# Kernel optimization log

Measured on AMD Instinct MI355X. Metric: run time of the kernel, lower is better.

## Reference

```python
import jax, jax.numpy as jnp
import numpy as np

B, T, I, H = 2048, 1024, 1, 20


def setup_inputs() -> dict:
    key = jax.random.key(0)
    ks = jax.random.split(key, 7)
    std = 0.01  # matches nn.init.normal_(p, mean=0.0, std=0.01)
    X = jax.random.normal(ks[0], (B, T, I), jnp.float32)
    hidden_prev = jnp.zeros((1, B, H), jnp.float32)
    W_ih = jax.random.normal(ks[1], (3 * H, I), jnp.float32) * std
    W_hh = jax.random.normal(ks[2], (3 * H, H), jnp.float32) * std
    b_ih = jax.random.normal(ks[3], (3 * H,), jnp.float32) * std
    b_hh = jax.random.normal(ks[4], (3 * H,), jnp.float32) * std
    W_out = jax.random.normal(ks[5], (1, H), jnp.float32) * std
    b_out = jax.random.normal(ks[6], (1,), jnp.float32) * std
    return dict(X=X, hidden_prev=hidden_prev, W_ih=W_ih, W_hh=W_hh,
                b_ih=b_ih, b_hh=b_hh, W_out=W_out, b_out=b_out)


def _gru(X, h0, W_ih, W_hh, b_ih, b_hh):
    # Precompute all input projections in one big GEMM: [T, B, 3H]
    gi = jnp.einsum('bti,gi->tbg', X, W_ih) + b_ih

    def step(h, gi_t):
        gh = h @ W_hh.T + b_hh                      # [B, 3H]
        i_r, i_z, i_n = jnp.split(gi_t, 3, axis=-1)  # PyTorch gate order: r, z, n
        h_r, h_z, h_n = jnp.split(gh, 3, axis=-1)
        r = jax.nn.sigmoid(i_r + h_r)
        z = jax.nn.sigmoid(i_z + h_z)
        n = jnp.tanh(i_n + r * h_n)
        h_new = (1.0 - z) * n + z * h
        return h_new, h_new

    h_last, outs = jax.lax.scan(step, h0, gi)        # outs: [T, B, H]
    return jnp.transpose(outs, (1, 0, 2)), h_last    # [B, T, H], [B, H]


def reference(X, hidden_prev, W_ih, W_hh, b_ih, b_hh, W_out, b_out):
    out, h_last = _gru(X, hidden_prev[0], W_ih, W_hh, b_ih, b_hh)
    y = out.reshape(-1, H) @ W_out.T + b_out         # [B*T, 1]
    return y[None], h_last[None]                     # [1, B*T, 1], [1, B, H]
```

## Files before the change

### kernel.cpp

```cpp
#include <hip/hip_runtime.h>


#define LOG2E 1.44269504088896340736f

static __device__ __forceinline__ float fast_rcp(float x) {
    return __builtin_amdgcn_rcpf(x);
}
static __device__ __forceinline__ float fast_exp2(float x) {
    float r;
    asm("v_exp_f32 %0, %1" : "=v"(r) : "v"(x));
    return r;
}
static __device__ __forceinline__ float lane_bcast(float v, int srclane) {
    return __int_as_float(__builtin_amdgcn_readlane(__float_as_int(v), srclane));
}

__global__ __launch_bounds__(64) void gru_fused(
    const float* __restrict__ X,
    const float* __restrict__ H0,
    const float* __restrict__ Wih,
    const float* __restrict__ Whh,
    const float* __restrict__ Bih,
    const float* __restrict__ Bhh,
    const float* __restrict__ Wout,
    const float* __restrict__ Bout,
    float* __restrict__ Y,
    float* __restrict__ Hlast)
{
    constexpr int T = 1024;
    constexpr int H = 20;
    const int b    = blockIdx.x;
    const int lane = threadIdx.x;

    __shared__ float lds[128];

    float w[H];
    float wih_full = 0.f, bihv = 0.f, cbias = 0.f, wih_rz = 0.f;
    if (lane < 60) {
        const float sc = (lane < 40) ? LOG2E : 2.0f * LOG2E;
        #pragma unroll
        for (int k = 0; k < H; ++k) w[k] = Whh[lane * H + k] * sc;
        wih_full = Wih[lane];
        bihv     = Bih[lane];
        if (lane < 40) {
            cbias  = (Bih[lane] + Bhh[lane]) * sc;
            wih_rz = wih_full * sc;
        } else {
            cbias     = Bhh[lane] * sc;
            wih_full *= sc;
            bihv     *= sc;
        }
    } else if (lane == 60) {
        #pragma unroll
        for (int k = 0; k < H; ++k) w[k] = Wout[k];
        cbias = Bout[0];
    } else {
        #pragma unroll
        for (int k = 0; k < H; ++k) w[k] = 0.f;
    }

    const bool is_n = (lane >= 40) && (lane < 60);
    const int  jn   = lane - 40;

    float hcur  = H0[b * H + (is_n ? jn : 0)];

    const int sr = is_n ? jn          : lane;
    const int sz = is_n ? (lane + -20) : lane;

    const float4* X4 = (const float4*)(X + (size_t)b * T);
    float4 xq = X4[0];

    for (int q = 0; q < T / 4; ++q) {
        float4 xn = X4[(q < T / 4 - 1) ? (q + 1) : (T / 4 - 1)];
        #pragma unroll
        for (int u = 0; u < 4; ++u) {
            const int   i = 4 * q + u;
            const float x = (u == 0) ? xq.x : (u == 1) ? xq.y
                          : (u == 2) ? xq.z : xq.w;

            if (u == 1 && (q & 15) == 0 && q > 0) {
                Y[(size_t)b * T + (4 * q - 64) + lane] = lds[lane];
            }

            float hs[H];
            #pragma unroll
            for (int k = 0; k < H; ++k) hs[k] = lane_bcast(hcur, 40 + k);

            float acc  = fmaf(x, wih_rz, cbias);
            float gi   = fmaf(x, wih_full, bihv);
            float acc2 = 0.f;
            #pragma unroll
            for (int k = 0; k < 10; ++k)  acc  = fmaf(hs[k], w[k], acc);
            #pragma unroll
            for (int k = 10; k < 20; ++k) acc2 = fmaf(hs[k], w[k], acc2);
            acc += acc2;

            float s = fast_rcp(1.f + fast_exp2(-acc));

            float rj = __shfl(s, sr, 64);
            float zj = __shfl(s, sz, 64);

            float npre = fmaf(rj, acc, gi);
            float nval = 1.f - 2.f * fast_rcp(1.f + fast_exp2(npre));
            float hnew = fmaf(zj, hcur - nval, nval);
            hcur = hnew;

            const int   waddr = (lane == 60) ? ((i + 63) & 63) : (64 + lane);
            const float wval  = (lane == 60) ? acc : 0.f;
            lds[waddr] = wval;
        }
        xq = xn;
    }

    {
        float hs[H];
        #pragma unroll
        for (int k = 0; k < H; ++k) hs[k] = lane_bcast(hcur, 40 + k);
        float acc  = cbias;
        float acc2 = 0.f;
        #pragma unroll
        for (int k = 0; k < 10; ++k)  acc  = fmaf(hs[k], w[k], acc);
        #pragma unroll
        for (int k = 10; k < 20; ++k) acc2 = fmaf(hs[k], w[k], acc2);
        acc += acc2;
        const int   waddr = (lane == 60) ? 63 : (64 + lane);
        const float wval  = (lane == 60) ? acc : 0.f;
        lds[waddr] = wval;
        Y[(size_t)b * T + (T - 64) + lane] = lds[lane];
    }

    if (is_n) Hlast[b * H + jn] = hcur;
}

extern "C" void kernel_launch(void* const* d_in, const int* in_sizes, int n_in,
                              void* d_out, int out_size, void* d_ws, size_t ws_size,
                              hipStream_t stream) {
    const float* X    = (const float*)d_in[0];
    const float* H0   = (const float*)d_in[1];
    const float* Wih  = (const float*)d_in[2];
    const float* Whh  = (const float*)d_in[3];
    const float* Bih  = (const float*)d_in[4];
    const float* Bhh  = (const float*)d_in[5];
    const float* Wout = (const float*)d_in[6];
    const float* Bout = (const float*)d_in[7];

    constexpr int B = 2048, T = 1024, H = 20;
    float* Y     = (float*)d_out;
    float* Hlast = Y + (size_t)B * T;

    gru_fused<<<dim3(B), dim3(64), 0, stream>>>(X, H0, Wih, Whh, Bih, Bhh,
                                                Wout, Bout, Y, Hlast);
}
```

Before: 309.7 us.

## Process two batch rows per wavefront to interleave independent GRU recurrences

Each 64-lane block now advances two independent batch sequences through the recurrence, issuing both steps back to back inside the unrolled inner loop. The grid is halved and the LDS staging buffer for Y grows to hold both sequences' outputs. The intent is to hide the serial latency of readlane broadcasts, exp/rcp and shuffles by giving the compiler two independent dependency chains per wave, instead of relying on the hardware to switch between two separate waves. The trade-off is higher register pressure, and fewer total waves, which may leave SIMDs with less latency hiding if the compiler does not interleave the two chains well.

```diff
diff --git a/kernel.cpp b/kernel.cpp
--- a/kernel.cpp
+++ b/kernel.cpp
@@ -15,7 +15,50 @@
     return __int_as_float(__builtin_amdgcn_readlane(__float_as_int(v), srclane));
 }
 
-__global__ __launch_bounds__(64) void gru_fused(
+static __device__ __forceinline__ float gru_step(
+    float x, float& hcur, const float* __restrict__ w,
+    float wih_rz, float wih_full, float bihv, float cbias,
+    int sr, int sz)
+{
+    float hs[20];
+    #pragma unroll
+    for (int k = 0; k < 20; ++k) hs[k] = lane_bcast(hcur, 40 + k);
+
+    float acc  = fmaf(x, wih_rz, cbias);
+    float gi   = fmaf(x, wih_full, bihv);
+    float acc2 = 0.f;
+    #pragma unroll
+    for (int k = 0; k < 10; ++k)  acc  = fmaf(hs[k], w[k], acc);
+    #pragma unroll
+    for (int k = 10; k < 20; ++k) acc2 = fmaf(hs[k], w[k], acc2);
+    acc += acc2;
+
+    float s  = fast_rcp(1.f + fast_exp2(-acc));
+    float rj = __shfl(s, sr, 64);
+    float zj = __shfl(s, sz, 64);
+
+    float npre = fmaf(rj, acc, gi);
+    float nval = 1.f - 2.f * fast_rcp(1.f + fast_exp2(npre));
+    hcur = fmaf(zj, hcur - nval, nval);
+    return acc;
+}
+
+static __device__ __forceinline__ float tail_dot(
+    float hcur, const float* __restrict__ w, float cbias)
+{
+    float hs[20];
+    #pragma unroll
+    for (int k = 0; k < 20; ++k) hs[k] = lane_bcast(hcur, 40 + k);
+    float acc  = cbias;
+    float acc2 = 0.f;
+    #pragma unroll
+    for (int k = 0; k < 10; ++k)  acc  = fmaf(hs[k], w[k], acc);
+    #pragma unroll
+    for (int k = 10; k < 20; ++k) acc2 = fmaf(hs[k], w[k], acc2);
+    return acc + acc2;
+}
+
+__global__ __launch_bounds__(64) void gru_fused2(
     const float* __restrict__ X,
     const float* __restrict__ H0,
     const float* __restrict__ Wih,
@@ -29,10 +72,11 @@
 {
     constexpr int T = 1024;
     constexpr int H = 20;
-    const int b    = blockIdx.x;
+    const int b0   = blockIdx.x * 2;
+    const int b1   = b0 + 1;
     const int lane = threadIdx.x;
 
-    __shared__ float lds[128];
+    __shared__ float lds[192];
 
     float w[H];
     float wih_full = 0.f, bihv = 0.f, cbias = 0.f, wih_rz = 0.f;
@@ -61,75 +105,60 @@
 
     const bool is_n = (lane >= 40) && (lane < 60);
     const int  jn   = lane - 40;
+    const int  sr   = is_n ? jn          : lane;
+    const int  sz   = is_n ? (lane - 20) : lane;
 
-    float hcur  = H0[b * H + (is_n ? jn : 0)];
+    float hA = H0[b0 * H + (is_n ? jn : 0)];
+    float hB = H0[b1 * H + (is_n ? jn : 0)];
 
-    const int sr = is_n ? jn          : lane;
-    const int sz = is_n ? (lane + -20) : lane;
+    const float4* X4A = (const float4*)(X + (size_t)b0 * T);
+    const float4* X4B = (const float4*)(X + (size_t)b1 * T);
+    float4 xqA = X4A[0], xqB = X4B[0];
 
-    const float4* X4 = (const float4*)(X + (size_t)b * T);
-    float4 xq = X4[0];
+    float* YA = Y + (size_t)b0 * T;
+    float* YB = Y + (size_t)b1 * T;
 
     for (int q = 0; q < T / 4; ++q) {
-        float4 xn = X4[(q < T / 4 - 1) ? (q + 1) : (T / 4 - 1)];
+        const int qn = (q < T / 4 - 1) ? (q + 1) : (T / 4 - 1);
+        float4 xnA = X4A[qn];
+        float4 xnB = X4B[qn];
         #pragma unroll
         for (int u = 0; u < 4; ++u) {
-            const int   i = 4 * q + u;
-            const float x = (u == 0) ? xq.x : (u == 1) ? xq.y
-                          : (u == 2) ? xq.z : xq.w;
+            const int   i  = 4 * q + u;
+            const float xA = (u == 0) ? xqA.x : (u == 1) ? xqA.y
+                           : (u == 2) ? xqA.z : xqA.w;
+            const float xB = (u == 0) ? xqB.x : (u == 1) ? xqB.y
+                           : (u == 2) ? xqB.z : xqB.w;
 
             if (u == 1 && (q & 15) == 0 && q > 0) {
-                Y[(size_t)b * T + (4 * q - 64) + lane] = lds[lane];
+                YA[(4 * q - 64) + lane] = lds[lane];
+                YB[(4 * q - 64) + lane] = lds[64 + lane];
             }
 
-            float hs[H];
-            #pragma unroll
-            for (int k = 0; k < H; ++k) hs[k] = lane_bcast(hcur, 40 + k);
+            float accA = gru_step(xA, hA, w, wih_rz, wih_full, bihv, cbias, sr, sz);
+            float accB = gru_step(xB, hB, w, wih_rz, wih_full, bihv, cbias, sr, sz);
 
-            float acc  = fmaf(x, wih_rz, cbias);
-            float gi   = fmaf(x, wih_full, bihv);
-            float acc2 = 0.f;
-            #pragma unroll
-            for (int k = 0; k < 10; ++k)  acc  = fmaf(hs[k], w[k], acc);
-            #pragma unroll
-            for (int k = 10; k < 20; ++k) acc2 = fmaf(hs[k], w[k], acc2);
-            acc += acc2;
-
-            float s = fast_rcp(1.f + fast_exp2(-acc));
-
-            float rj = __shfl(s, sr, 64);
-            float zj = __shfl(s, sz, 64);
-
-            float npre = fmaf(rj, acc, gi);
-            float nval = 1.f - 2.f * fast_rcp(1.f + fast_exp2(npre));
-            float hnew = fmaf(zj, hcur - nval, nval);
-            hcur = hnew;
-
-            const int   waddr = (lane == 60) ? ((i + 63) & 63) : (64 + lane);
-            const float wval  = (lane == 60) ? acc : 0.f;
-            lds[waddr] = wval;
+            const int slot = (i + 63) & 63;
+            lds[(lane == 60) ? slot        : (128 + lane)] = accA;
+            lds[(lane == 60) ? (64 + slot) : (128 + lane)] = accB;
         }
-        xq = xn;
+        xqA = xnA;
+        xqB = xnB;
     }
 
     {
-        float hs[H];
-        #pragma unroll
-        for (int k = 0; k < H; ++k) hs[k] = lane_bcast(hcur, 40 + k);
-        float acc  = cbias;
-        float acc2 = 0.f;
-        #pragma unroll
-        for (int k = 0; k < 10; ++k)  acc  = fmaf(hs[k], w[k], acc);
-        #pragma unroll
-        for (int k = 10; k < 20; ++k) acc2 = fmaf(hs[k], w[k], acc2);
-        acc += acc2;
-        const int   waddr = (lane == 60) ? 63 : (64 + lane);
-        const float wval  = (lane == 60) ? acc : 0.f;
-        lds[waddr] = wval;
-        Y[(size_t)b * T + (T - 64) + lane] = lds[lane];
+        float accA = tail_dot(hA, w, cbias);
+        float accB = tail_dot(hB, w, cbias);
+        lds[(lane == 60) ? 63  : (128 + lane)] = accA;
+        lds[(lane == 60) ? 127 : (128 + lane)] = accB;
+        YA[(T - 64) + lane] = lds[lane];
+        YB[(T - 64) + lane] = lds[64 + lane];
     }
 
-    if (is_n) Hlast[b * H + jn] = hcur;
+    if (is_n) {
+        Hlast[b0 * H + jn] = hA;
+        Hlast[b1 * H + jn] = hB;
+    }
 }
 
 extern "C" void kernel_launch(void* const* d_in, const int* in_sizes, int n_in,
@@ -148,6 +177,6 @@
     float* Y     = (float*)d_out;
     float* Hlast = Y + (size_t)B * T;
 
-    gru_fused<<<dim3(B), dim3(64), 0, stream>>>(X, H0, Wih, Whh, Bih, Bhh,
-                                                Wout, Bout, Y, Hlast);
+    gru_fused2<<<dim3(B / 2), dim3(64), 0, stream>>>(X, H0, Wih, Whh, Bih, Bhh,
+                                                     Wout, Bout, Y, Hlast);
 }
```

After: 351.3 us. +13.4%, slower.

## Pack r/n and z/Wout gate rows into paired lanes using v_pk_fma_f32

Applied to the files above, without the earlier changes.

Each lane now holds two gate rows as float2 weight pairs: r with n in lanes 0-19, and z with the output projection in lanes 32-51. The recurrent matvec uses packed FP32 FMAs with the broadcast hidden state duplicated into SGPR pairs, and the accumulation is split across four chains. This removes one of the two cross-lane shuffles per step and shortens the serial critical path per timestep. The cost is hand-written inline asm and a more complex lane mapping, so correctness depends on the lane-to-gate index arithmetic being right.

```diff
diff --git a/kernel.cpp b/kernel.cpp
--- a/kernel.cpp
+++ b/kernel.cpp
@@ -3,19 +3,43 @@
 
 #define LOG2E 1.44269504088896340736f
 
+typedef float f32x2 __attribute__((ext_vector_type(2)));
+
 static __device__ __forceinline__ float fast_rcp(float x) {
     return __builtin_amdgcn_rcpf(x);
 }
-static __device__ __forceinline__ float fast_exp2(float x) {
-    float r;
-    asm("v_exp_f32 %0, %1" : "=v"(r) : "v"(x));
-    return r;
+static __device__ __forceinline__ float exp2neg(float x) {
+    float r; asm("v_exp_f32 %0, -%1" : "=v"(r) : "v"(x)); return r;
 }
-static __device__ __forceinline__ float lane_bcast(float v, int srclane) {
-    return __int_as_float(__builtin_amdgcn_readlane(__float_as_int(v), srclane));
+static __device__ __forceinline__ float exp2pos(float x) {
+    float r; asm("v_exp_f32 %0, %1" : "=v"(r) : "v"(x)); return r;
+}
+static __device__ __forceinline__ unsigned long long dup_sgpr(unsigned int u) {
+    return (((unsigned long long)u) << 32) | (unsigned long long)u;
+}
+static __device__ __forceinline__ void pk_fma_acc(f32x2& acc, f32x2 w,
+                                                  unsigned long long hp) {
+    asm("v_pk_fma_f32 %0, %1, %2, %0" : "+v"(acc) : "v"(w), "s"(hp));
+}
+static __device__ __forceinline__ f32x2 pk_mul(f32x2 w, unsigned long long hp) {
+    f32x2 d; asm("v_pk_mul_f32 %0, %1, %2" : "=v"(d) : "v"(w), "s"(hp));
+    return d;
+}
+static __device__ __forceinline__ f32x2 pk_fma3(f32x2 xf, unsigned long long xp,
+                                                f32x2 cb) {
+    f32x2 d;
+    asm("v_pk_fma_f32 %0, %1, %2, %3" : "=v"(d) : "v"(xf), "s"(xp), "v"(cb));
+    return d;
+}
+static __device__ __forceinline__ f32x2 pk_add(f32x2 a, f32x2 b) {
+    f32x2 d; asm("v_pk_add_f32 %0, %1, %2" : "=v"(d) : "v"(a), "v"(b));
+    return d;
+}
+static __device__ __forceinline__ int rfl(float v) {
+    return __builtin_amdgcn_readfirstlane(__float_as_int(v));
 }
 
-__global__ __launch_bounds__(64) void gru_fused(
+__global__ __launch_bounds__(64) void gru_pk(
     const float* __restrict__ X,
     const float* __restrict__ H0,
     const float* __restrict__ Wih,
@@ -34,102 +58,117 @@
 
     __shared__ float lds[128];
 
-    float w[H];
-    float wih_full = 0.f, bihv = 0.f, cbias = 0.f, wih_rz = 0.f;
-    if (lane < 60) {
-        const float sc = (lane < 40) ? LOG2E : 2.0f * LOG2E;
+    f32x2 w[H];
+    f32x2 cb = {0.f, 0.f}, xf = {0.f, 0.f};
+    float wihn2 = 0.f, bihn2 = 0.f;
+    if (lane < 20) {
         #pragma unroll
-        for (int k = 0; k < H; ++k) w[k] = Whh[lane * H + k] * sc;
-        wih_full = Wih[lane];
-        bihv     = Bih[lane];
-        if (lane < 40) {
-            cbias  = (Bih[lane] + Bhh[lane]) * sc;
-            wih_rz = wih_full * sc;
-        } else {
-            cbias     = Bhh[lane] * sc;
-            wih_full *= sc;
-            bihv     *= sc;
-        }
-    } else if (lane == 60) {
+        for (int k = 0; k < H; ++k)
+            w[k] = f32x2{Whh[lane * H + k] * LOG2E,
+                         Whh[(40 + lane) * H + k] * (2.f * LOG2E)};
+        cb    = f32x2{(Bih[lane] + Bhh[lane]) * LOG2E,
+                      Bhh[40 + lane] * (2.f * LOG2E)};
+        xf    = f32x2{Wih[lane] * LOG2E, 0.f};
+        wihn2 = Wih[40 + lane] * (2.f * LOG2E);
+        bihn2 = Bih[40 + lane] * (2.f * LOG2E);
+    } else if (lane >= 32 && lane < 52) {
+        const int j = lane - 32;
         #pragma unroll
-        for (int k = 0; k < H; ++k) w[k] = Wout[k];
-        cbias = Bout[0];
+        for (int k = 0; k < H; ++k)
+            w[k] = f32x2{Whh[(20 + j) * H + k] * LOG2E,
+                         (j == 0) ? Wout[k] : 0.f};
+        cb = f32x2{(Bih[20 + j] + Bhh[20 + j]) * LOG2E,
+                   (j == 0) ? Bout[0] : 0.f};
+        xf = f32x2{Wih[20 + j] * LOG2E, 0.f};
     } else {
         #pragma unroll
-        for (int k = 0; k < H; ++k) w[k] = 0.f;
+        for (int k = 0; k < H; ++k) w[k] = f32x2{0.f, 0.f};
     }
 
-    const bool is_n = (lane >= 40) && (lane < 60);
-    const int  jn   = lane - 40;
+    const bool isy = (lane == 32);
+    const int  ztr = (lane < 32) ? (lane + 32) : lane;
 
-    float hcur  = H0[b * H + (is_n ? jn : 0)];
-
-    const int sr = is_n ? jn          : lane;
-    const int sz = is_n ? (lane + -20) : lane;
+    float hcur = H0[b * H + ((lane < 20) ? lane : 0)];
 
     const float4* X4 = (const float4*)(X + (size_t)b * T);
     float4 xq = X4[0];
 
     for (int q = 0; q < T / 4; ++q) {
-        float4 xn = X4[(q < T / 4 - 1) ? (q + 1) : (T / 4 - 1)];
+        const int qn = (q < T / 4 - 1) ? (q + 1) : (T / 4 - 1);
+        float4 xn = X4[qn];
         #pragma unroll
         for (int u = 0; u < 4; ++u) {
-            const int   i = 4 * q + u;
-            const float x = (u == 0) ? xq.x : (u == 1) ? xq.y
-                          : (u == 2) ? xq.z : xq.w;
+            const int   i  = 4 * q + u;
+            const float xv = (u == 0) ? xq.x : (u == 1) ? xq.y
+                           : (u == 2) ? xq.z : xq.w;
 
             if (u == 1 && (q & 15) == 0 && q > 0) {
                 Y[(size_t)b * T + (4 * q - 64) + lane] = lds[lane];
             }
 
-            float hs[H];
+            const unsigned int      xu = (unsigned int)rfl(xv);
+            const unsigned long long xp = dup_sgpr(xu);
+
+            unsigned long long hp[H];
             #pragma unroll
-            for (int k = 0; k < H; ++k) hs[k] = lane_bcast(hcur, 40 + k);
+            for (int k = 0; k < H; ++k)
+                hp[k] = dup_sgpr(
+                    (unsigned int)__builtin_amdgcn_readlane(
+                        __float_as_int(hcur), k));
 
-            float acc  = fmaf(x, wih_rz, cbias);
-            float gi   = fmaf(x, wih_full, bihv);
-            float acc2 = 0.f;
+            f32x2 a0 = pk_fma3(xf, xp, cb);
+            f32x2 a1 = pk_mul(w[1], hp[1]);
+            f32x2 a2 = pk_mul(w[2], hp[2]);
+            f32x2 a3 = pk_mul(w[3], hp[3]);
+            pk_fma_acc(a0, w[0], hp[0]);
             #pragma unroll
-            for (int k = 0; k < 10; ++k)  acc  = fmaf(hs[k], w[k], acc);
-            #pragma unroll
-            for (int k = 10; k < 20; ++k) acc2 = fmaf(hs[k], w[k], acc2);
-            acc += acc2;
+            for (int k = 4; k < H; k += 4) {
+                pk_fma_acc(a0, w[k],     hp[k]);
+                pk_fma_acc(a1, w[k + 1], hp[k + 1]);
+                pk_fma_acc(a2, w[k + 2], hp[k + 2]);
+                pk_fma_acc(a3, w[k + 3], hp[k + 3]);
+            }
+            const f32x2 acc = pk_add(pk_add(a0, a1), pk_add(a2, a3));
 
-            float s = fast_rcp(1.f + fast_exp2(-acc));
+            const float s = fast_rcp(1.f + exp2neg(acc.x));
+            const float zj = __shfl(s, ztr, 64);
 
-            float rj = __shfl(s, sr, 64);
-            float zj = __shfl(s, sz, 64);
+            const float gi   = fmaf(xv, wihn2, bihn2);
+            const float npre = fmaf(s, acc.y, gi);
+            const float nval = fmaf(fast_rcp(1.f + exp2pos(npre)), -2.f, 1.f);
+            hcur = fmaf(zj, hcur - nval, nval);
 
-            float npre = fmaf(rj, acc, gi);
-            float nval = 1.f - 2.f * fast_rcp(1.f + fast_exp2(npre));
-            float hnew = fmaf(zj, hcur - nval, nval);
-            hcur = hnew;
-
-            const int   waddr = (lane == 60) ? ((i + 63) & 63) : (64 + lane);
-            const float wval  = (lane == 60) ? acc : 0.f;
-            lds[waddr] = wval;
+            const int waddr = isy ? ((i + 63) & 63) : (64 + lane);
+            lds[waddr] = acc.y;
         }
         xq = xn;
     }
 
     {
-        float hs[H];
+        unsigned long long hp[H];
         #pragma unroll
-        for (int k = 0; k < H; ++k) hs[k] = lane_bcast(hcur, 40 + k);
-        float acc  = cbias;
-        float acc2 = 0.f;
+        for (int k = 0; k < H; ++k)
+            hp[k] = dup_sgpr(
+                (unsigned int)__builtin_amdgcn_readlane(
+                    __float_as_int(hcur), k));
+        f32x2 a0 = cb;
+        f32x2 a1 = pk_mul(w[1], hp[1]);
+        f32x2 a2 = pk_mul(w[2], hp[2]);
+        f32x2 a3 = pk_mul(w[3], hp[3]);
+        pk_fma_acc(a0, w[0], hp[0]);
         #pragma unroll
-        for (int k = 0; k < 10; ++k)  acc  = fmaf(hs[k], w[k], acc);
-        #pragma unroll
-        for (int k = 10; k < 20; ++k) acc2 = fmaf(hs[k], w[k], acc2);
-        acc += acc2;
-        const int   waddr = (lane == 60) ? 63 : (64 + lane);
-        const float wval  = (lane == 60) ? acc : 0.f;
-        lds[waddr] = wval;
+        for (int k = 4; k < H; k += 4) {
+            pk_fma_acc(a0, w[k],     hp[k]);
+            pk_fma_acc(a1, w[k + 1], hp[k + 1]);
+            pk_fma_acc(a2, w[k + 2], hp[k + 2]);
+            pk_fma_acc(a3, w[k + 3], hp[k + 3]);
+        }
+        const f32x2 acc = pk_add(pk_add(a0, a1), pk_add(a2, a3));
+        lds[isy ? 63 : (64 + lane)] = acc.y;
         Y[(size_t)b * T + (T - 64) + lane] = lds[lane];
     }
 
-    if (is_n) Hlast[b * H + jn] = hcur;
+    if (lane < 20) Hlast[b * H + lane] = hcur;
 }
 
 extern "C" void kernel_launch(void* const* d_in, const int* in_sizes, int n_in,
@@ -148,6 +187,6 @@
     float* Y     = (float*)d_out;
     float* Hlast = Y + (size_t)B * T;
 
-    gru_fused<<<dim3(B), dim3(64), 0, stream>>>(X, H0, Wih, Whh, Bih, Bhh,
-                                                Wout, Bout, Y, Hlast);
+    gru_pk<<<dim3(B), dim3(64), 0, stream>>>(X, H0, Wih, Whh, Bih, Bhh,
+                                             Wout, Bout, Y, Hlast);
 }
```

Measured after the change: 387.4 us. +25.1%, slower.

## Remap gate lanes so r-gate exchange uses permlane32 swap, split dot product

Applied to the files above, without the earlier changes.

Reassigns the gate rows to wavefront lanes so each n-gate lane (32-51) sits exactly 32 lanes above its r-gate lane. The r value can then be fetched with v_permlane32_swap instead of a ds_bpermute shuffle, which shortens the serial per-timestep dependency chain. The 20-term hidden dot product is also split into four independent accumulators to expose more ILP, and the exp negation is folded into the instruction operand. The z-gate still uses a shuffle, and the lane-mapping changes add index arithmetic that must stay consistent with the broadcast lanes.

```diff
diff --git a/kernel.cpp b/kernel.cpp
--- a/kernel.cpp
+++ b/kernel.cpp
@@ -6,16 +6,22 @@
 static __device__ __forceinline__ float fast_rcp(float x) {
     return __builtin_amdgcn_rcpf(x);
 }
-static __device__ __forceinline__ float fast_exp2(float x) {
-    float r;
-    asm("v_exp_f32 %0, %1" : "=v"(r) : "v"(x));
-    return r;
+static __device__ __forceinline__ float exp2neg(float x) {
+    float r; asm("v_exp_f32 %0, -%1" : "=v"(r) : "v"(x)); return r;
+}
+static __device__ __forceinline__ float exp2pos(float x) {
+    float r; asm("v_exp_f32 %0, %1" : "=v"(r) : "v"(x)); return r;
 }
 static __device__ __forceinline__ float lane_bcast(float v, int srclane) {
     return __int_as_float(__builtin_amdgcn_readlane(__float_as_int(v), srclane));
 }
+static __device__ __forceinline__ float swap_up(float v) {
+    float d = v, s = v;
+    asm("v_permlane32_swap_b32 %0, %1" : "+v"(d), "+v"(s));
+    return s;
+}
 
-__global__ __launch_bounds__(64) void gru_fused(
+__global__ __launch_bounds__(64) void gru_pl(
     const float* __restrict__ X,
     const float* __restrict__ H0,
     const float* __restrict__ Wih,
@@ -34,22 +40,25 @@
 
     __shared__ float lds[128];
 
+    const bool is_n  = (lane >= 32) && (lane < 52);
+    const bool is_rz = (lane < 32) || (lane >= 52 && lane < 60);
+    const int row = (lane < 32) ? lane
+                  : (lane < 52) ? (lane + 8)
+                  : (lane < 60) ? (lane - 20) : 0;
+
     float w[H];
     float wih_full = 0.f, bihv = 0.f, cbias = 0.f, wih_rz = 0.f;
-    if (lane < 60) {
-        const float sc = (lane < 40) ? LOG2E : 2.0f * LOG2E;
+    if (is_rz) {
         #pragma unroll
-        for (int k = 0; k < H; ++k) w[k] = Whh[lane * H + k] * sc;
-        wih_full = Wih[lane];
-        bihv     = Bih[lane];
-        if (lane < 40) {
-            cbias  = (Bih[lane] + Bhh[lane]) * sc;
-            wih_rz = wih_full * sc;
-        } else {
-            cbias     = Bhh[lane] * sc;
-            wih_full *= sc;
-            bihv     *= sc;
-        }
+        for (int k = 0; k < H; ++k) w[k] = Whh[row * H + k] * LOG2E;
+        cbias  = (Bih[row] + Bhh[row]) * LOG2E;
+        wih_rz = Wih[row] * LOG2E;
+    } else if (is_n) {
+        #pragma unroll
+        for (int k = 0; k < H; ++k) w[k] = Whh[row * H + k] * (2.f * LOG2E);
+        cbias    = Bhh[row] * (2.f * LOG2E);
+        wih_full = Wih[row] * (2.f * LOG2E);
+        bihv     = Bih[row] * (2.f * LOG2E);
     } else if (lane == 60) {
         #pragma unroll
         for (int k = 0; k < H; ++k) w[k] = Wout[k];
@@ -59,24 +68,22 @@
         for (int k = 0; k < H; ++k) w[k] = 0.f;
     }
 
-    const bool is_n = (lane >= 40) && (lane < 60);
-    const int  jn   = lane - 40;
+    const int jn = lane - 32;
+    const int sz = is_n ? ((lane < 44) ? (lane - 12) : (lane + 8)) : lane;
 
-    float hcur  = H0[b * H + (is_n ? jn : 0)];
-
-    const int sr = is_n ? jn          : lane;
-    const int sz = is_n ? (lane + -20) : lane;
+    float hcur = H0[b * H + (is_n ? jn : 0)];
 
     const float4* X4 = (const float4*)(X + (size_t)b * T);
     float4 xq = X4[0];
 
     for (int q = 0; q < T / 4; ++q) {
-        float4 xn = X4[(q < T / 4 - 1) ? (q + 1) : (T / 4 - 1)];
+        const int qn = (q < T / 4 - 1) ? (q + 1) : (T / 4 - 1);
+        float4 xn = X4[qn];
         #pragma unroll
         for (int u = 0; u < 4; ++u) {
-            const int   i = 4 * q + u;
-            const float x = (u == 0) ? xq.x : (u == 1) ? xq.y
-                          : (u == 2) ? xq.z : xq.w;
+            const int   i  = 4 * q + u;
+            const float xv = (u == 0) ? xq.x : (u == 1) ? xq.y
+                           : (u == 2) ? xq.z : xq.w;
 
             if (u == 1 && (q & 15) == 0 && q > 0) {
                 Y[(size_t)b * T + (4 * q - 64) + lane] = lds[lane];
@@ -84,30 +91,33 @@
 
             float hs[H];
             #pragma unroll
-            for (int k = 0; k < H; ++k) hs[k] = lane_bcast(hcur, 40 + k);
+            for (int k = 0; k < H; ++k) hs[k] = lane_bcast(hcur, 32 + k);
 
-            float acc  = fmaf(x, wih_rz, cbias);
-            float gi   = fmaf(x, wih_full, bihv);
-            float acc2 = 0.f;
+            float a0 = fmaf(xv, wih_rz, cbias);
+            float gi = fmaf(xv, wih_full, bihv);
+            float a1 = hs[1] * w[1];
+            float a2 = hs[2] * w[2];
+            float a3 = hs[3] * w[3];
+            a0 = fmaf(hs[0], w[0], a0);
             #pragma unroll
-            for (int k = 0; k < 10; ++k)  acc  = fmaf(hs[k], w[k], acc);
-            #pragma unroll
-            for (int k = 10; k < 20; ++k) acc2 = fmaf(hs[k], w[k], acc2);
-            acc += acc2;
+            for (int k = 4; k < H; k += 4) {
+                a0 = fmaf(hs[k],     w[k],     a0);
+                a1 = fmaf(hs[k + 1], w[k + 1], a1);
+                a2 = fmaf(hs[k + 2], w[k + 2], a2);
+                a3 = fmaf(hs[k + 3], w[k + 3], a3);
+            }
+            const float acc = (a0 + a1) + (a2 + a3);
 
-            float s = fast_rcp(1.f + fast_exp2(-acc));
+            const float s = fast_rcp(1.f + exp2neg(acc));
 
-            float rj = __shfl(s, sr, 64);
-            float zj = __shfl(s, sz, 64);
+            const float rj = swap_up(s);
+            const float zj = __shfl(s, sz, 64);
 
-            float npre = fmaf(rj, acc, gi);
-            float nval = 1.f - 2.f * fast_rcp(1.f + fast_exp2(npre));
-            float hnew = fmaf(zj, hcur - nval, nval);
-            hcur = hnew;
+            const float npre = fmaf(rj, acc, gi);
+            const float nval = fmaf(fast_rcp(1.f + exp2pos(npre)), -2.f, 1.f);
+            hcur = fmaf(zj, hcur - nval, nval);
 
-            const int   waddr = (lane == 60) ? ((i + 63) & 63) : (64 + lane);
-            const float wval  = (lane == 60) ? acc : 0.f;
-            lds[waddr] = wval;
+            lds[(lane == 60) ? ((i + 63) & 63) : (64 + lane)] = acc;
         }
         xq = xn;
     }
@@ -115,17 +125,21 @@
     {
         float hs[H];
         #pragma unroll
-        for (int k = 0; k < H; ++k) hs[k] = lane_bcast(hcur, 40 + k);
-        float acc  = cbias;
-        float acc2 = 0.f;
+        for (int k = 0; k < H; ++k) hs[k] = lane_bcast(hcur, 32 + k);
+        float a0 = cbias;
+        float a1 = hs[1] * w[1];
+        float a2 = hs[2] * w[2];
+        float a3 = hs[3] * w[3];
+        a0 = fmaf(hs[0], w[0], a0);
         #pragma unroll
-        for (int k = 0; k < 10; ++k)  acc  = fmaf(hs[k], w[k], acc);
-        #pragma unroll
-        for (int k = 10; k < 20; ++k) acc2 = fmaf(hs[k], w[k], acc2);
-        acc += acc2;
-        const int   waddr = (lane == 60) ? 63 : (64 + lane);
-        const float wval  = (lane == 60) ? acc : 0.f;
-        lds[waddr] = wval;
+        for (int k = 4; k < H; k += 4) {
+            a0 = fmaf(hs[k],     w[k],     a0);
+            a1 = fmaf(hs[k + 1], w[k + 1], a1);
+            a2 = fmaf(hs[k + 2], w[k + 2], a2);
+            a3 = fmaf(hs[k + 3], w[k + 3], a3);
+        }
+        const float acc = (a0 + a1) + (a2 + a3);
+        lds[(lane == 60) ? 63 : (64 + lane)] = acc;
         Y[(size_t)b * T + (T - 64) + lane] = lds[lane];
     }
 
@@ -148,6 +162,6 @@
     float* Y     = (float*)d_out;
     float* Hlast = Y + (size_t)B * T;
 
-    gru_fused<<<dim3(B), dim3(64), 0, stream>>>(X, H0, Wih, Whh, Bih, Bhh,
-                                                Wout, Bout, Y, Hlast);
+    gru_pl<<<dim3(B), dim3(64), 0, stream>>>(X, H0, Wih, Whh, Bih, Bhh,
+                                             Wout, Bout, Y, Hlast);
 }
```

Result: no change. 307.8 us (-0.6%).
